# Kernel optimization log

Hardware: AMD Instinct MI355X
Metric: run time of the kernel (lower is better)

The kernel has to match this reference:

```python
import jax, jax.numpy as jnp
import numpy as np

B, S, D, H = 16, 512, 1024, 4096
TOP_K = H // 4  # default: hidden_dim // 4


def setup_inputs() -> dict:
    key = jax.random.key(0)
    ks = jax.random.split(key, 11)
    s = lambda fan_in: 1.0 / np.sqrt(fan_in)
    return {
        "inputs": jax.random.normal(ks[0], (B, S, D), jnp.float32),
        "up_w": jax.random.uniform(ks[1], (H, D), jnp.float32, -s(D), s(D)),
        "up_b": jax.random.uniform(ks[2], (H,), jnp.float32, -s(D), s(D)),
        "gate_w1": jax.random.uniform(ks[3], (H, D), jnp.float32, -s(D), s(D)),
        "gate_b1": jax.random.uniform(ks[4], (H,), jnp.float32, -s(D), s(D)),
        "gate_w2": jax.random.uniform(ks[5], (H, H), jnp.float32, -s(H), s(H)),
        "gate_b2": jax.random.uniform(ks[6], (H,), jnp.float32, -s(H), s(H)),
        "mod_w": jax.random.uniform(ks[7], (H, D), jnp.float32, -s(D), s(D)),
        "mod_b": jax.random.uniform(ks[8], (H,), jnp.float32, -s(D), s(D)),
        "down_w": jax.random.uniform(ks[9], (D, H), jnp.float32, -s(H), s(H)),
        "down_b": jax.random.uniform(ks[10], (D,), jnp.float32, -s(H), s(H)),
    }


def reference(inputs, up_w, up_b, gate_w1, gate_b1, gate_w2, gate_b2,
              mod_w, mod_b, down_w, down_b):
    b, s_len, d = inputs.shape
    h_dim = up_w.shape[0]
    # gate MLP -> scores [B, S, H]
    scores = jax.nn.relu(jnp.einsum('bsd,hd->bsh', inputs, gate_w1) + gate_b1)
    scores = jnp.einsum('bsh,gh->bsg', scores, gate_w2) + gate_b2
    flat = scores.reshape(b, s_len * h_dim)
    k = min(TOP_K * s_len, s_len * h_dim)
    _, flat_idx = jax.lax.top_k(flat, k)                    # [B, k]
    hidden_idx = flat_idx % h_dim                           # [B, k]
    # mask[b, h] = True if row h of up.weight was overwritten by mod.weight
    # (duplicate indices write the same value, so set-semantics are exact)
    mask = jnp.zeros((b, h_dim), bool).at[
        jnp.arange(b)[:, None], hidden_idx].set(True)       # [B, H]
    # Instead of materializing per-batch [B,H,D] weights, compute both shared-
    # weight GEMMs and select per (batch, hidden) row — identical math.
    h_up = jnp.einsum('bsd,hd->bsh', inputs, up_w) + up_b
    h_mod = jnp.einsum('bsd,hd->bsh', inputs, mod_w) + mod_b
    h = jnp.where(mask[:, None, :], h_mod, h_up)            # [B, S, H]
    h = jax.nn.silu(h)
    # dropout is identity in eval/reference mode
    return jnp.einsum('bsh,dh->bsd', h, down_w) + down_b
```

## Files before the change

kernel.cpp:

```cpp
#include <hip/hip_runtime.h>
#include <cstdint>

typedef __attribute__((ext_vector_type(4))) _Float16 f16x4;
typedef __attribute__((ext_vector_type(8))) _Float16 f16x8;
typedef __attribute__((ext_vector_type(4))) float f32x4;

#define D_DIM 1024
#define H_DIM 4096
#define BS_ROWS 8192
#define K_SEL 524288u
#define CAND_CAP 32768u

__device__ __forceinline__ unsigned lkey(float v){
  float u = fmaf(v, 67108864.f, 268435456.f);
  u = fminf(fmaxf(u, 0.f), 536870911.f);
  return (unsigned)u;
}

__device__ __forceinline__ void gload16(const _Float16* g, _Float16* l){
  __builtin_amdgcn_global_load_lds(
      (const __attribute__((address_space(1))) void*)g,
      (__attribute__((address_space(3))) void*)l, 16, 0, 0);
}

template<int N> __device__ __forceinline__ void waitcnt_vm(){
  if      constexpr (N == 0) asm volatile("s_waitcnt vmcnt(0)" ::: "memory");
  else if constexpr (N == 4) asm volatile("s_waitcnt vmcnt(4)" ::: "memory");
  else if constexpr (N == 6) asm volatile("s_waitcnt vmcnt(6)" ::: "memory");
  else                       asm volatile("s_waitcnt vmcnt(8)" ::: "memory");
}

__device__ __forceinline__ size_t img_g32(int row, int k8, int nkt32){
  int p = (row & 127) >> 1;
  int s = (((row & 1) << 2) | (k8 & 3)) ^ (p & 7);
  return ((size_t)((row >> 7) * nkt32 + (k8 >> 2)) << 9) + (p << 3) + s;
}

__global__ __launch_bounds__(256)
void pack_all(const float* __restrict__ X, const float* __restrict__ g1w,
              const float* __restrict__ g2w, const float* __restrict__ upw,
              const float* __restrict__ modw, const float* __restrict__ dww,
              _Float16* __restrict__ Xhi, _Float16* __restrict__ Xlo,
              _Float16* __restrict__ G1hi, _Float16* __restrict__ G1lo,
              _Float16* __restrict__ G2hi, _Float16* __restrict__ G2lo,
              _Float16* __restrict__ UPhi, _Float16* __restrict__ MODhi,
              _Float16* __restrict__ DWhi)
{
  unsigned g = blockIdx.x * 256u + threadIdx.x;
  const float* W; _Float16* hi; _Float16* lo = nullptr;
  int k8s, n32; unsigned base;
  if      (g < 1048576u){ W=X;    hi=Xhi;  lo=Xlo;  k8s=7; n32=32;  base=0u;        }
  else if (g < 1572864u){ W=g1w;  hi=G1hi; lo=G1lo; k8s=7; n32=32;  base=1048576u; }
  else if (g < 3670016u){ W=g2w;  hi=G2hi; lo=G2lo; k8s=9; n32=128; base=1572864u; }
  else if (g < 4194304u){ W=upw;  hi=UPhi;          k8s=7; n32=32;  base=3670016u; }
  else if (g < 4718592u){ W=modw; hi=MODhi;         k8s=7; n32=32;  base=4194304u; }
  else                  { W=dww;  hi=DWhi;          k8s=9; n32=128; base=4718592u; }
  g -= base;
  int row = (int)(g >> k8s), k8 = (int)(g & ((1u << k8s) - 1u));
  const float* src = W + ((size_t)row << (k8s + 3)) + (k8 << 3);
  float4 f0 = *(const float4*)src, f1 = *(const float4*)(src + 4);
  float ff[8] = {f0.x,f0.y,f0.z,f0.w,f1.x,f1.y,f1.z,f1.w};
  f16x8 hv, lv;
  #pragma unroll
  for (int i = 0; i < 8; i++){
    hv[i] = (_Float16)ff[i];
    lv[i] = (_Float16)(ff[i] - (float)hv[i]);
  }
  size_t d = img_g32(row, k8, n32) << 3;
  *(f16x8*)&hi[d] = hv;
  if (lo) *(f16x8*)&lo[d] = lv;
}

enum { MODE_G1 = 0, MODE_G2 = 1, MODE_UPMOD = 2, MODE_DOWN = 3 };

template<int MODE>
__global__ __launch_bounds__(256)
void gemm_t(const _Float16* __restrict__ Ahi, const _Float16* __restrict__ Alo,
            const _Float16* __restrict__ Bhi, const _Float16* __restrict__ Blo,
            const float* __restrict__ bias0, const float* __restrict__ bias1,
            const unsigned* __restrict__ mask,
            _Float16* __restrict__ Chi, _Float16* __restrict__ Clo,
            float* __restrict__ C32,
            int N, int K, int m_img_base, int c_row_base)
{
  constexpr int NSEG = (MODE == MODE_G1) ? 3 : 1;
  constexpr bool BSEL = (MODE == MODE_UPMOD);
  constexpr int NLD = (NSEG == 3) ? 8 : 4;
  constexpr int DEPTH = (NSEG == 3) ? 2 : 3;
  __shared__ __align__(16) _Float16 sA [DEPTH][4096];
  __shared__ __align__(16) _Float16 sB [DEPTH][4096];
  __shared__ __align__(16) _Float16 sAl[NSEG == 3 ? 2 : 1][NSEG == 3 ? 4096 : 8];
  __shared__ __align__(16) _Float16 sBl[NSEG == 3 ? 2 : 1][NSEG == 3 ? 4096 : 8];

  const int nbx = gridDim.x;
  const int h = blockIdx.y * nbx + blockIdx.x;
  const int xcd = h & 7, idx = h >> 3;
  const int cw = nbx >> 2;
  const int ch = gridDim.y >> 1;
  const int bx = (xcd & 3) * cw + idx % cw;
  const int by = (xcd >> 2) * ch + idx / cw;

  const int tid = threadIdx.x;
  const int lane = tid & 63;
  const int w  = tid >> 6;
  const int wr = w >> 1, wc = w & 1;
  const int lr = lane & 15;
  const int q  = lane >> 4;

  const int m0 = m_img_base + by * 128;
  const int n0 = bx * 128;
  const int nkt = K >> 5;
  const size_t arow = (size_t)(m0 >> 7) * nkt;
  const size_t brow = (size_t)(n0 >> 7) * nkt;

  const _Float16* bsrcl[2];
  if (BSEL){
    const int bb = m0 >> 9;
    #pragma unroll
    for (int j = 0; j < 2; j++){
      int gi = (w*2 + j)*64 + lane;
      int p = gi >> 3, x = (gi & 7) ^ (p & 7);
      int row = (p << 1) | (x >> 2);
      bsrcl[j] = (mask[bb * H_DIM + n0 + row] ? Blo : Bhi) + (gi << 3);
    }
    waitcnt_vm<0>();
  }

  f32x4 acc[4][4];
  #pragma unroll
  for (int i = 0; i < 4; i++)
    #pragma unroll
    for (int j = 0; j < 4; j++) acc[i][j] = (f32x4){0.f,0.f,0.f,0.f};

  const int soff = (((((lr & 1) << 2) | q) ^ (lr >> 1)) << 3);

  auto STAGE = [&](int buf, int kt){
    const _Float16* at = Ahi + ((arow + kt) << 12);
    #pragma unroll
    for (int j = 0; j < 2; j++)
      gload16(at + ((w*2 + j) << 9) + (lane << 3), &sA[buf][(w*2 + j) << 9]);
    if (NSEG == 3){
      const _Float16* alt = Alo + ((arow + kt) << 12);
      const _Float16* bht = Bhi + ((brow + kt) << 12);
      const _Float16* blt = Blo + ((brow + kt) << 12);
      #pragma unroll
      for (int j = 0; j < 2; j++){
        gload16(alt + ((w*2 + j) << 9) + (lane << 3), &sAl[buf][(w*2 + j) << 9]);
        gload16(bht + ((w*2 + j) << 9) + (lane << 3), &sB [buf][(w*2 + j) << 9]);
        gload16(blt + ((w*2 + j) << 9) + (lane << 3), &sBl[buf][(w*2 + j) << 9]);
      }
    } else if (BSEL){
      const size_t toff = (brow + kt) << 12;
      #pragma unroll
      for (int j = 0; j < 2; j++)
        gload16(bsrcl[j] + toff, &sB[buf][(w*2 + j) << 9]);
    } else {
      const _Float16* bht = Bhi + ((brow + kt) << 12);
      #pragma unroll
      for (int j = 0; j < 2; j++)
        gload16(bht + ((w*2 + j) << 9) + (lane << 3), &sB[buf][(w*2 + j) << 9]);
    }
  };

  STAGE(0, 0);
  if (DEPTH == 3) STAGE(1, 1);

  for (int kt = 0; kt < nkt; ++kt){
    const int rem = nkt - 1 - kt;
    const int cur = (DEPTH == 2) ? (kt & 1) : (kt % 3);
    if (DEPTH == 2){
      if (rem >= 1){ STAGE((kt + 1) & 1, kt + 1); waitcnt_vm<NLD>(); }
      else         { waitcnt_vm<0>(); }
    } else {
      if (rem >= 2){ STAGE((kt + 2) % 3, kt + 2); waitcnt_vm<8>(); }
      else if (rem == 1){ waitcnt_vm<4>(); }
      else         { waitcnt_vm<0>(); }
    }
    __builtin_amdgcn_s_barrier();
    __builtin_amdgcn_sched_barrier(0);

    f16x8 fah[4], fbh[4], fal[4], fbl[4];
    #pragma unroll
    for (int i = 0; i < 4; i++){
      const int ap = ((wr*32 + i*8 + (lr >> 1)) << 6) + soff;
      const int bp = ((wc*32 + i*8 + (lr >> 1)) << 6) + soff;
      fah[i] = *(const f16x8*)&sA[cur][ap];
      fbh[i] = *(const f16x8*)&sB[cur][bp];
      if (NSEG == 3){
        fal[i] = *(const f16x8*)&sAl[cur][ap];
        fbl[i] = *(const f16x8*)&sBl[cur][bp];
      }
    }
    #pragma unroll
    for (int mi = 0; mi < 4; mi++)
      #pragma unroll
      for (int ni = 0; ni < 4; ni++)
        acc[mi][ni] = __builtin_amdgcn_mfma_f32_16x16x32_f16(fah[mi], fbh[ni], acc[mi][ni], 0,0,0);
    if (NSEG == 3){
      #pragma unroll
      for (int mi = 0; mi < 4; mi++)
        #pragma unroll
        for (int ni = 0; ni < 4; ni++)
          acc[mi][ni] = __builtin_amdgcn_mfma_f32_16x16x32_f16(fal[mi], fbh[ni], acc[mi][ni], 0,0,0);
      #pragma unroll
      for (int mi = 0; mi < 4; mi++)
        #pragma unroll
        for (int ni = 0; ni < 4; ni++)
          acc[mi][ni] = __builtin_amdgcn_mfma_f32_16x16x32_f16(fah[mi], fbl[ni], acc[mi][ni], 0,0,0);
    }
    __builtin_amdgcn_s_barrier();
  }

  #pragma unroll
  for (int ni = 0; ni < 4; ni++){
    const int gc = n0 + wc*64 + ni*16 + lr;
    float bias;
    if (MODE == MODE_UPMOD) bias = mask[(m0 >> 9) * H_DIM + gc] ? bias1[gc] : bias0[gc];
    else                    bias = bias0[gc];
    #pragma unroll
    for (int mi = 0; mi < 4; mi++){
      #pragma unroll
      for (int r = 0; r < 4; r++){
        const int gr = m0 + wr*64 + mi*16 + q*4 + r;
        const int cr = gr - c_row_base;
        float v = acc[mi][ni][r] + bias;
        if (MODE == MODE_G1){
          v = fmaxf(v, 0.f);
          size_t d = (img_g32(cr, gc >> 3, N >> 5) << 3) + (gc & 7);
          Chi[d] = (_Float16)v;
        }
        if (MODE == MODE_UPMOD){
          v = v / (1.f + __expf(-v));
          size_t d = (img_g32(cr, gc >> 3, N >> 5) << 3) + (gc & 7);
          Chi[d] = (_Float16)v;
        }
        if (MODE == MODE_DOWN) C32[(size_t)cr * N + gc] = v;
      }
    }
  }
}

__global__ __launch_bounds__(512, 1)
void gemm_g1(const _Float16* __restrict__ Ahi, const _Float16* __restrict__ Alo,
             const _Float16* __restrict__ Bhi, const _Float16* __restrict__ Blo,
             const float* __restrict__ bias0, _Float16* __restrict__ Chi,
             int N, int K, int m_img_base, int c_row_base)
{
  __shared__ __align__(16) _Float16 sAh[3][8192];
  __shared__ __align__(16) _Float16 sAl[3][8192];
  __shared__ __align__(16) _Float16 sBh[3][4096];
  __shared__ __align__(16) _Float16 sBl[3][4096];

  const int nbx = gridDim.x;
  const int h = blockIdx.y * nbx + blockIdx.x;
  const int xcd = h & 7, idx = h >> 3;
  const int cw = nbx >> 2, ch = gridDim.y >> 1;
  const int bx = (xcd & 3) * cw + idx % cw;
  const int by = (xcd >> 2) * ch + idx / cw;

  const int tid = threadIdx.x;
  const int lane = tid & 63;
  const int w = tid >> 6;
  const int wrow = w >> 1, wcol = w & 1;
  const int lr = lane & 15;
  const int q = lane >> 4;

  const int m0 = m_img_base + by * 256;
  const int n0 = bx * 128;
  const int nkt = K >> 5;
  const int at0 = (m0 >> 7) * nkt;
  const int bt0 = (n0 >> 7) * nkt;

  f32x4 acc[4][4];
  #pragma unroll
  for (int i = 0; i < 4; i++)
    #pragma unroll
    for (int j = 0; j < 4; j++) acc[i][j] = (f32x4){0.f,0.f,0.f,0.f};

  const int soff = (((((lr & 1) << 2) | q) ^ (lr >> 1)) << 3);
  int offA[4], offB[4];
  #pragma unroll
  for (int mi = 0; mi < 4; mi++)
    offA[mi] = (wrow >> 1)*4096 + ((((wrow & 1)*32) + mi*8 + (lr >> 1)) << 6) + soff;
  #pragma unroll
  for (int ni = 0; ni < 4; ni++)
    offB[ni] = ((wcol*32 + ni*8 + (lr >> 1)) << 6) + soff;

  auto STA = [&](int buf, int rb, int kt, bool lo){
    const _Float16* img = lo ? Alo : Ahi;
    _Float16* dst = (lo ? &sAl[buf][0] : &sAh[buf][0]) + rb*4096 + (tid << 3);
    gload16(img + ((((size_t)(at0 + rb*nkt + kt)) << 9) + tid) * 8, dst);
  };
  auto STB = [&](int buf, int kt, bool lo){
    const _Float16* img = lo ? Blo : Bhi;
    _Float16* dst = (lo ? &sBl[buf][0] : &sBh[buf][0]) + (tid << 3);
    gload16(img + ((((size_t)(bt0 + kt)) << 9) + tid) * 8, dst);
  };

#define G1PHASE(P, STG)                                                        \
  {                                                                            \
    f16x8 ah = *(const f16x8*)&sAh[cur][offA[P]];                              \
    f16x8 al = *(const f16x8*)&sAl[cur][offA[P]];                              \
    STG;                                                                       \
    if ((P) == 3){ if (pf) waitcnt_vm<6>(); else waitcnt_vm<0>(); }            \
    __builtin_amdgcn_s_barrier();                                              \
    asm volatile("s_waitcnt lgkmcnt(0)" ::: "memory");                         \
    __builtin_amdgcn_sched_barrier(0);                                         \
    __builtin_amdgcn_s_setprio(1);                                             \
    _Pragma("unroll")                                                          \
    for (int ni = 0; ni < 4; ni++)                                             \
      acc[P][ni] = __builtin_amdgcn_mfma_f32_16x16x32_f16(ah, fbh[ni], acc[P][ni], 0,0,0); \
    _Pragma("unroll")                                                          \
    for (int ni = 0; ni < 4; ni++)                                             \
      acc[P][ni] = __builtin_amdgcn_mfma_f32_16x16x32_f16(al, fbh[ni], acc[P][ni], 0,0,0); \
    _Pragma("unroll")                                                          \
    for (int ni = 0; ni < 4; ni++)                                             \
      acc[P][ni] = __builtin_amdgcn_mfma_f32_16x16x32_f16(ah, fbl[ni], acc[P][ni], 0,0,0); \
    __builtin_amdgcn_s_setprio(0);                                             \
    __builtin_amdgcn_s_barrier();                                              \
  }

  STA(0,0,0,false); STA(0,1,0,false); STA(0,0,0,true); STA(0,1,0,true);
  STB(0,0,false);   STB(0,0,true);
  STA(1,0,1,false); STA(1,1,1,false); STA(1,0,1,true); STA(1,1,1,true);
  STB(1,1,false);   STB(1,1,true);
  waitcnt_vm<6>();
  __builtin_amdgcn_s_barrier();

  for (int kt = 0; kt < nkt; ++kt){
    const int cur = kt % 3, nb = (kt + 2) % 3;
    const bool pf = (kt + 2 < nkt);
    f16x8 fbh[4], fbl[4];
    #pragma unroll
    for (int ni = 0; ni < 4; ni++){
      fbh[ni] = *(const f16x8*)&sBh[cur][offB[ni]];
      fbl[ni] = *(const f16x8*)&sBl[cur][offB[ni]];
    }
    G1PHASE(0, if (pf){ STA(nb,0,kt+2,false); STA(nb,1,kt+2,false); })
    G1PHASE(1, if (pf){ STA(nb,0,kt+2,true);  STA(nb,1,kt+2,true);  })
    G1PHASE(2, if (pf){ STB(nb,kt+2,false);   STB(nb,kt+2,true);    })
    G1PHASE(3, )
  }
#undef G1PHASE

  #pragma unroll
  for (int ni = 0; ni < 4; ni++){
    const int gc = n0 + wcol*64 + ni*16 + lr;
    const float bias = bias0[gc];
    #pragma unroll
    for (int mi = 0; mi < 4; mi++){
      #pragma unroll
      for (int r = 0; r < 4; r++){
        const int gr = m0 + wrow*64 + mi*16 + q*4 + r;
        const int cr = gr - c_row_base;
        float v = fmaxf(acc[mi][ni][r] + bias, 0.f);
        size_t d = (img_g32(cr, gc >> 3, N >> 5) << 3) + (gc & 7);
        Chi[d] = (_Float16)v;
      }
    }
  }
}

__global__ __launch_bounds__(512, 2)
void gemm_g2(const _Float16* __restrict__ A, const _Float16* __restrict__ B,
             const float* __restrict__ bias0,
             unsigned* __restrict__ keys, unsigned* __restrict__ Mkey,
             unsigned* __restrict__ hist, int N, int K, int batch_base)
{
  __shared__ __align__(16) _Float16 sAb[3][8192];
  __shared__ __align__(16) _Float16 sBb[3][8192];

  const int nbx = gridDim.x;
  const int h = blockIdx.y * nbx + blockIdx.x;
  const int xcd = h & 7, idx = h >> 3;
  const int cw = nbx >> 2, ch = gridDim.y >> 1;
  const int bx = (xcd & 3) * cw + idx % cw;
  const int by = (xcd >> 2) * ch + idx / cw;

  const int tid = threadIdx.x;
  const int lane = tid & 63;
  const int w = tid >> 6;
  const int wrow = w >> 2, wcol = w & 3;
  const int lr = lane & 15;
  const int q = lane >> 4;

  const int m0 = by * 256;
  const int n0 = bx * 256;
  const int nkt = K >> 5;
  const int ar0 = (m0 >> 7) * nkt;
  const int br0 = (n0 >> 7) * nkt;

  f32x4 acc[8][4];
  #pragma unroll
  for (int i = 0; i < 8; i++)
    #pragma unroll
    for (int j = 0; j < 4; j++) acc[i][j] = (f32x4){0.f,0.f,0.f,0.f};

  const int soff = (((((lr & 1) << 2) | q) ^ (lr >> 1)) << 3);
  int offA[8], offB[4];
  #pragma unroll
  for (int mi = 0; mi < 8; mi++) offA[mi] = ((mi*8 + (lr >> 1)) << 6) + soff;
  #pragma unroll
  for (int ni = 0; ni < 4; ni++)
    offB[ni] = (((wcol & 1)*32 + ni*8 + (lr >> 1)) << 6) + soff;
  const int arb = wrow * 4096;
  const int bcb = (wcol >> 1) * 4096;

  auto STA = [&](int buf, int rb, int kt){
    gload16(A + ((((size_t)(ar0 + rb*nkt + kt) << 9) + tid) << 3),
            &sAb[buf][rb*4096 + (tid << 3)]);
  };
  auto STB = [&](int buf, int cb, int kt){
    gload16(B + ((((size_t)(br0 + cb*nkt + kt) << 9) + tid) << 3),
            &sBb[buf][cb*4096 + (tid << 3)]);
  };

#define G2PHASE(P, STG)                                                        \
  {                                                                            \
    f16x8 a0 = *(const f16x8*)&sAb[cur][arb + offA[2*(P)]];                    \
    f16x8 a1 = *(const f16x8*)&sAb[cur][arb + offA[2*(P)+1]];                  \
    STG;                                                                       \
    if ((P) == 3){ if (pf) waitcnt_vm<4>(); else waitcnt_vm<0>(); }            \
    __builtin_amdgcn_s_barrier();                                              \
    asm volatile("s_waitcnt lgkmcnt(0)" ::: "memory");                         \
    __builtin_amdgcn_sched_barrier(0);                                         \
    __builtin_amdgcn_s_setprio(1);                                             \
    _Pragma("unroll")                                                          \
    for (int ni = 0; ni < 4; ni++)                                             \
      acc[2*(P)][ni]   = __builtin_amdgcn_mfma_f32_16x16x32_f16(a0, fb[ni], acc[2*(P)][ni], 0,0,0);   \
    _Pragma("unroll")                                                          \
    for (int ni = 0; ni < 4; ni++)                                             \
      acc[2*(P)+1][ni] = __builtin_amdgcn_mfma_f32_16x16x32_f16(a1, fb[ni], acc[2*(P)+1][ni], 0,0,0); \
    __builtin_amdgcn_s_setprio(0);                                             \
    __builtin_amdgcn_s_barrier();                                              \
  }

  STA(0,0,0); STB(0,0,0); STB(0,1,0); STA(0,1,0);
  STA(1,0,1); STB(1,0,1); STB(1,1,1); STA(1,1,1);
  waitcnt_vm<4>();
  __builtin_amdgcn_s_barrier();

  for (int kt = 0; kt < nkt; ++kt){
    const int cur = kt % 3, nb = (kt + 2) % 3;
    const bool pf = (kt + 2 < nkt);
    f16x8 fb[4];
    #pragma unroll
    for (int ni = 0; ni < 4; ni++)
      fb[ni] = *(const f16x8*)&sBb[cur][bcb + offB[ni]];
    G2PHASE(0, if (pf) STA(nb, 0, kt+2))
    G2PHASE(1, if (pf) STB(nb, 0, kt+2))
    G2PHASE(2, if (pf) STB(nb, 1, kt+2))
    G2PHASE(3, if (pf) STA(nb, 1, kt+2))
  }
#undef G2PHASE

  unsigned* lh = (unsigned*)&sAb[0][0];
  __syncthreads();
  for (int i = tid; i < 4096; i += 512) lh[i] = 0;
  __syncthreads();

  const int gb = batch_base + (m0 >> 9);
  #pragma unroll
  for (int ni = 0; ni < 4; ni++){
    const int gc = n0 + wcol*64 + ni*16 + lr;
    const float bias = bias0[gc];
    unsigned colmax = 0u;
    #pragma unroll
    for (int mi = 0; mi < 8; mi++){
      #pragma unroll
      for (int r = 0; r < 4; r++){
        const int gr = m0 + wrow*128 + mi*16 + q*4 + r;
        float v = acc[mi][ni][r] + bias;
        unsigned key = lkey(v);
        keys[(size_t)gr * N + gc] = key;
        colmax = max(colmax, key);
        atomicAdd(&lh[key >> 17], 1u);
      }
    }
    atomicMax(&Mkey[gb * H_DIM + gc], colmax);
  }
  __syncthreads();
  for (int i = tid; i < 4096; i += 512)
    if (lh[i]) atomicAdd(&hist[(gb << 12) + i], lh[i]);
}


__global__ __launch_bounds__(256)
void select12(const unsigned* __restrict__ hist, unsigned* __restrict__ b12,
              unsigned* __restrict__ krem, unsigned* __restrict__ ccount, int b0)
{
  const int b = b0 + (int)blockIdx.x;
  __shared__ unsigned part[256];
  const unsigned base = (unsigned)b << 12;
  unsigned s = 0;
  #pragma unroll
  for (int i = 0; i < 16; i++) s += hist[base + threadIdx.x*16 + i];
  part[threadIdx.x] = s;
  __syncthreads();
  if (threadIdx.x == 0){
    unsigned cum = 0; int t = 255;
    for (; t > 0; --t){
      if (cum + part[t] >= K_SEL) break;
      cum += part[t];
    }
    int bin = 15; unsigned kr = K_SEL;
    for (; bin > 0; --bin){
      unsigned c = hist[base + t*16 + bin];
      if (cum + c >= K_SEL) break;
      cum += c;
    }
    kr = K_SEL - cum;
    b12[b] = (unsigned)(t*16 + bin);
    krem[b] = kr;
    ccount[b] = 0;
  }
}

__global__ __launch_bounds__(256)
void collect(const unsigned* __restrict__ keys, const unsigned* __restrict__ b12,
             unsigned* __restrict__ cand, unsigned* __restrict__ ccount, int b0)
{
  __shared__ unsigned cbuf[1024];
  __shared__ unsigned lcnt, gbase;
  const int bl = blockIdx.y;
  const int b  = b0 + bl;
  const unsigned bin = b12[b];
  if (threadIdx.x == 0) lcnt = 0;
  __syncthreads();
  const uint4* p = (const uint4*)(keys + (size_t)bl*2097152u + (size_t)blockIdx.x*8192u);
  uint4 kv[8];
  #pragma unroll
  for (int j = 0; j < 8; j++) kv[j] = p[threadIdx.x + j*256];
  #pragma unroll
  for (int j = 0; j < 8; j++){
    #pragma unroll
    for (int e = 0; e < 4; e++){
      unsigned k = (e==0)?kv[j].x:(e==1)?kv[j].y:(e==2)?kv[j].z:kv[j].w;
      if ((k >> 17) == bin){
        unsigned idx = atomicAdd(&lcnt, 1u);
        if (idx < 1024u) cbuf[idx] = k;
      }
    }
  }
  __syncthreads();
  const unsigned n = lcnt < 1024u ? lcnt : 1024u;
  if (threadIdx.x == 0) gbase = atomicAdd(&ccount[b], n);
  __syncthreads();
  const unsigned gb = gbase;
  for (unsigned i = threadIdx.x; i < n; i += 256){
    unsigned dst = gb + i;
    if (dst < CAND_CAP) cand[((size_t)b << 15) + dst] = cbuf[i];
  }
}

__global__ __launch_bounds__(256)
void select_exact(const unsigned* __restrict__ cand, const unsigned* __restrict__ ccount,
                  const unsigned* __restrict__ b12, const unsigned* __restrict__ kremA,
                  unsigned* __restrict__ tkey, int b0)
{
  const int b = b0 + (int)blockIdx.x;
  unsigned cc = ccount[b];
  const unsigned n = cc < CAND_CAP ? cc : CAND_CAP;
  __shared__ unsigned h[256];
  __shared__ unsigned sh2[2];
  unsigned prefix = b12[b] << 17;
  unsigned krem = kremA[b];
  const unsigned pm[3]  = {0xFFFE0000u, 0xFFFFFE00u, 0xFFFFFFFEu};
  const int      shs[3] = {9, 1, 0};
  const int      wid[3] = {256, 256, 2};
  for (int pass = 0; pass < 3; ++pass){
    if (threadIdx.x < (unsigned)wid[pass]) h[threadIdx.x] = 0;
    __syncthreads();
    for (unsigned i = threadIdx.x; i < n; i += 256){
      unsigned k = cand[((size_t)b << 15) + i];
      if ((k & pm[pass]) == prefix)
        atomicAdd(&h[(k >> shs[pass]) & (unsigned)(wid[pass]-1)], 1u);
    }
    __syncthreads();
    if (threadIdx.x == 0){
      unsigned cum = 0; int bin = wid[pass]-1;
      for (; bin > 0; --bin){
        unsigned c = h[bin];
        if (cum + c >= krem) break;
        cum += c;
      }
      krem -= cum;
      prefix |= ((unsigned)bin) << shs[pass];
      sh2[0] = prefix; sh2[1] = krem;
    }
    __syncthreads();
    prefix = sh2[0]; krem = sh2[1];
    __syncthreads();
  }
  if (threadIdx.x == 0) tkey[b] = prefix;
}

__global__ __launch_bounds__(256)
void make_mask(const unsigned* __restrict__ Mkey, const unsigned* __restrict__ tkey,
               unsigned* __restrict__ mask){
  const int i = blockIdx.x * 256 + threadIdx.x;
  const int b = i >> 12;
  mask[i] = (Mkey[i] >= tkey[b]) ? 1u : 0u;
}

extern "C" void kernel_launch(void* const* d_in, const int* in_sizes, int n_in,
                              void* d_out, int out_size, void* d_ws, size_t ws_size,
                              hipStream_t stream)
{
  (void)in_sizes; (void)n_in; (void)out_size; (void)ws_size;
  const float* X      = (const float*)d_in[0];
  const float* up_w   = (const float*)d_in[1];
  const float* up_b   = (const float*)d_in[2];
  const float* g1w    = (const float*)d_in[3];
  const float* g1b    = (const float*)d_in[4];
  const float* g2w    = (const float*)d_in[5];
  const float* g2b    = (const float*)d_in[6];
  const float* mod_w  = (const float*)d_in[7];
  const float* mod_b  = (const float*)d_in[8];
  const float* down_w = (const float*)d_in[9];
  const float* down_b = (const float*)d_in[10];
  float* out = (float*)d_out;

  char* ws = (char*)d_ws;
  _Float16* Xhi  = (_Float16*)(ws);
  _Float16* Xlo  = (_Float16*)(ws + (16ull<<20));
  _Float16* G1hi = (_Float16*)(ws + (32ull<<20));
  _Float16* G1lo = (_Float16*)(ws + (40ull<<20));
  _Float16* G2hi = (_Float16*)(ws + (48ull<<20));
  _Float16* UPhi = (_Float16*)(ws + (112ull<<20));
  _Float16* MODhi= (_Float16*)(ws + (120ull<<20));
  _Float16* DWhi = (_Float16*)(ws + (128ull<<20));
  _Float16* Fhi  = (_Float16*)(ws + (136ull<<20));
  unsigned* keys = (unsigned*)(ws + (168ull<<20));
  _Float16* Hbuf = (_Float16*)(ws + (136ull<<20));
  char* aux = ws + (232ull<<20);
  unsigned* Mkey  = (unsigned*)(aux);
  unsigned* maskb = (unsigned*)(aux + 262144);
  unsigned* hist  = (unsigned*)(aux + 524288);
  unsigned* cand  = (unsigned*)(aux + 786432);
  unsigned* b12   = (unsigned*)(aux + 786432 + 2097152);
  unsigned* krem  = (unsigned*)(aux + 786432 + 2097152 + 64);
  unsigned* ccnt  = (unsigned*)(aux + 786432 + 2097152 + 128);
  unsigned* tkey  = (unsigned*)(aux + 786432 + 2097152 + 192);

  pack_all<<<20480, 256, 0, stream>>>(X, g1w, g2w, up_w, mod_w, down_w,
                                      Xhi, Xlo, G1hi, G1lo, G2hi, nullptr,
                                      UPhi, MODhi, DWhi);

  hipMemsetAsync(Mkey, 0, 262144, stream);
  hipMemsetAsync(hist, 0, 262144, stream);

  for (int half = 0; half < 2; ++half){
    const int b0 = half * 8;
    gemm_g1<<<dim3(32, 16), 512, 0, stream>>>(
        Xhi, Xlo, G1hi, G1lo, g1b, Fhi, H_DIM, D_DIM, half*4096, half*4096);
    gemm_g2<<<dim3(16, 16), 512, 0, stream>>>(
        Fhi, G2hi, g2b, keys, Mkey, hist, H_DIM, H_DIM, b0);
    select12<<<8, 256, 0, stream>>>(hist, b12, krem, ccnt, b0);
    collect<<<dim3(256, 8), 256, 0, stream>>>(keys, b12, cand, ccnt, b0);
    select_exact<<<8, 256, 0, stream>>>(cand, ccnt, b12, krem, tkey, b0);
  }
  make_mask<<<256, 256, 0, stream>>>(Mkey, tkey, maskb);

  gemm_t<MODE_UPMOD><<<dim3(32, 64), 256, 0, stream>>>(
      Xhi, nullptr, UPhi, MODhi, up_b, mod_b, maskb,
      Hbuf, nullptr, nullptr, H_DIM, D_DIM, 0, 0);
  gemm_t<MODE_DOWN><<<dim3(8, 64), 256, 0, stream>>>(
      Hbuf, nullptr, DWhi, nullptr, down_b, nullptr, nullptr,
      nullptr, nullptr, out, D_DIM, H_DIM, 0, 0);
}
```

Measured before the change: 934.2 us.

## Restructure gate-1 split-fp16 GEMM as virtual 3x-K loop with 256x256 tiles

```diff
diff --git a/kernel.cpp b/kernel.cpp
--- a/kernel.cpp
+++ b/kernel.cpp
@@ -241,15 +241,13 @@
 }
 
 __global__ __launch_bounds__(512, 1)
-void gemm_g1(const _Float16* __restrict__ Ahi, const _Float16* __restrict__ Alo,
-             const _Float16* __restrict__ Bhi, const _Float16* __restrict__ Blo,
-             const float* __restrict__ bias0, _Float16* __restrict__ Chi,
-             int N, int K, int m_img_base, int c_row_base)
-{
-  __shared__ __align__(16) _Float16 sAh[3][8192];
-  __shared__ __align__(16) _Float16 sAl[3][8192];
-  __shared__ __align__(16) _Float16 sBh[3][4096];
-  __shared__ __align__(16) _Float16 sBl[3][4096];
+void gemm_g1v(const _Float16* __restrict__ Ahi, const _Float16* __restrict__ Alo,
+              const _Float16* __restrict__ Bhi, const _Float16* __restrict__ Blo,
+              const float* __restrict__ bias0, _Float16* __restrict__ Chi,
+              int N, int K, int m_img_base, int c_row_base)
+{
+  __shared__ __align__(16) _Float16 sAb[3][8192];
+  __shared__ __align__(16) _Float16 sBb[3][8192];
 
   const int nbx = gridDim.x;
   const int h = blockIdx.y * nbx + blockIdx.x;
@@ -261,97 +259,94 @@
   const int tid = threadIdx.x;
   const int lane = tid & 63;
   const int w = tid >> 6;
-  const int wrow = w >> 1, wcol = w & 1;
+  const int wrow = w >> 2, wcol = w & 3;
   const int lr = lane & 15;
   const int q = lane >> 4;
 
   const int m0 = m_img_base + by * 256;
-  const int n0 = bx * 128;
-  const int nkt = K >> 5;
-  const int at0 = (m0 >> 7) * nkt;
-  const int bt0 = (n0 >> 7) * nkt;
-
-  f32x4 acc[4][4];
-  #pragma unroll
-  for (int i = 0; i < 4; i++)
+  const int n0 = bx * 256;
+  const int nks = K >> 5;
+  const int nkt = 3 * nks;
+  const int ar0 = (m0 >> 7) * nks;
+  const int br0 = (n0 >> 7) * nks;
+
+  f32x4 acc[8][4];
+  #pragma unroll
+  for (int i = 0; i < 8; i++)
     #pragma unroll
     for (int j = 0; j < 4; j++) acc[i][j] = (f32x4){0.f,0.f,0.f,0.f};
 
   const int soff = (((((lr & 1) << 2) | q) ^ (lr >> 1)) << 3);
-  int offA[4], offB[4];
-  #pragma unroll
-  for (int mi = 0; mi < 4; mi++)
-    offA[mi] = (wrow >> 1)*4096 + ((((wrow & 1)*32) + mi*8 + (lr >> 1)) << 6) + soff;
+  int offA[8], offB[4];
+  #pragma unroll
+  for (int mi = 0; mi < 8; mi++) offA[mi] = ((mi*8 + (lr >> 1)) << 6) + soff;
   #pragma unroll
   for (int ni = 0; ni < 4; ni++)
-    offB[ni] = ((wcol*32 + ni*8 + (lr >> 1)) << 6) + soff;
-
-  auto STA = [&](int buf, int rb, int kt, bool lo){
-    const _Float16* img = lo ? Alo : Ahi;
-    _Float16* dst = (lo ? &sAl[buf][0] : &sAh[buf][0]) + rb*4096 + (tid << 3);
-    gload16(img + ((((size_t)(at0 + rb*nkt + kt)) << 9) + tid) * 8, dst);
+    offB[ni] = (((wcol & 1)*32 + ni*8 + (lr >> 1)) << 6) + soff;
+  const int arb = wrow * 4096;
+  const int bcb = (wcol >> 1) * 4096;
+
+  auto STA = [&](int buf, int rb, int kt){
+    const int seg = kt >> 5, lk = kt & 31;
+    const _Float16* img = (seg == 1) ? Alo : Ahi;
+    gload16(img + ((((size_t)(ar0 + rb*nks + lk) << 9) + tid) << 3),
+            &sAb[buf][rb*4096 + (tid << 3)]);
   };
-  auto STB = [&](int buf, int kt, bool lo){
-    const _Float16* img = lo ? Blo : Bhi;
-    _Float16* dst = (lo ? &sBl[buf][0] : &sBh[buf][0]) + (tid << 3);
-    gload16(img + ((((size_t)(bt0 + kt)) << 9) + tid) * 8, dst);
+  auto STB = [&](int buf, int cb, int kt){
+    const int seg = kt >> 5, lk = kt & 31;
+    const _Float16* img = (seg == 2) ? Blo : Bhi;
+    gload16(img + ((((size_t)(br0 + cb*nks + lk) << 9) + tid) << 3),
+            &sBb[buf][cb*4096 + (tid << 3)]);
   };
 
-#define G1PHASE(P, STG)                                                        \
+#define G1VPHASE(P, STG)                                                       \
   {                                                                            \
-    f16x8 ah = *(const f16x8*)&sAh[cur][offA[P]];                              \
-    f16x8 al = *(const f16x8*)&sAl[cur][offA[P]];                              \
+    f16x8 a0 = *(const f16x8*)&sAb[cur][arb + offA[2*(P)]];                    \
+    f16x8 a1 = *(const f16x8*)&sAb[cur][arb + offA[2*(P)+1]];                  \
     STG;                                                                       \
-    if ((P) == 3){ if (pf) waitcnt_vm<6>(); else waitcnt_vm<0>(); }            \
+    if ((P) == 3){ if (pf) waitcnt_vm<4>(); else waitcnt_vm<0>(); }            \
     __builtin_amdgcn_s_barrier();                                              \
     asm volatile("s_waitcnt lgkmcnt(0)" ::: "memory");                         \
     __builtin_amdgcn_sched_barrier(0);                                         \
     __builtin_amdgcn_s_setprio(1);                                             \
     _Pragma("unroll")                                                          \
     for (int ni = 0; ni < 4; ni++)                                             \
-      acc[P][ni] = __builtin_amdgcn_mfma_f32_16x16x32_f16(ah, fbh[ni], acc[P][ni], 0,0,0); \
+      acc[2*(P)][ni]   = __builtin_amdgcn_mfma_f32_16x16x32_f16(a0, fb[ni], acc[2*(P)][ni], 0,0,0);   \
     _Pragma("unroll")                                                          \
     for (int ni = 0; ni < 4; ni++)                                             \
-      acc[P][ni] = __builtin_amdgcn_mfma_f32_16x16x32_f16(al, fbh[ni], acc[P][ni], 0,0,0); \
-    _Pragma("unroll")                                                          \
-    for (int ni = 0; ni < 4; ni++)                                             \
-      acc[P][ni] = __builtin_amdgcn_mfma_f32_16x16x32_f16(ah, fbl[ni], acc[P][ni], 0,0,0); \
+      acc[2*(P)+1][ni] = __builtin_amdgcn_mfma_f32_16x16x32_f16(a1, fb[ni], acc[2*(P)+1][ni], 0,0,0); \
     __builtin_amdgcn_s_setprio(0);                                             \
     __builtin_amdgcn_s_barrier();                                              \
   }
 
-  STA(0,0,0,false); STA(0,1,0,false); STA(0,0,0,true); STA(0,1,0,true);
-  STB(0,0,false);   STB(0,0,true);
-  STA(1,0,1,false); STA(1,1,1,false); STA(1,0,1,true); STA(1,1,1,true);
-  STB(1,1,false);   STB(1,1,true);
-  waitcnt_vm<6>();
+  STA(0,0,0); STB(0,0,0); STB(0,1,0); STA(0,1,0);
+  STA(1,0,1); STB(1,0,1); STB(1,1,1); STA(1,1,1);
+  waitcnt_vm<4>();
   __builtin_amdgcn_s_barrier();
 
   for (int kt = 0; kt < nkt; ++kt){
     const int cur = kt % 3, nb = (kt + 2) % 3;
     const bool pf = (kt + 2 < nkt);
-    f16x8 fbh[4], fbl[4];
-    #pragma unroll
-    for (int ni = 0; ni < 4; ni++){
-      fbh[ni] = *(const f16x8*)&sBh[cur][offB[ni]];
-      fbl[ni] = *(const f16x8*)&sBl[cur][offB[ni]];
-    }
-    G1PHASE(0, if (pf){ STA(nb,0,kt+2,false); STA(nb,1,kt+2,false); })
-    G1PHASE(1, if (pf){ STA(nb,0,kt+2,true);  STA(nb,1,kt+2,true);  })
-    G1PHASE(2, if (pf){ STB(nb,kt+2,false);   STB(nb,kt+2,true);    })
-    G1PHASE(3, )
-  }
-#undef G1PHASE
+    f16x8 fb[4];
+    #pragma unroll
+    for (int ni = 0; ni < 4; ni++)
+      fb[ni] = *(const f16x8*)&sBb[cur][bcb + offB[ni]];
+    G1VPHASE(0, if (pf) STA(nb, 0, kt+2))
+    G1VPHASE(1, if (pf) STB(nb, 0, kt+2))
+    G1VPHASE(2, if (pf) STB(nb, 1, kt+2))
+    G1VPHASE(3, if (pf) STA(nb, 1, kt+2))
+  }
+#undef G1VPHASE
 
   #pragma unroll
   for (int ni = 0; ni < 4; ni++){
     const int gc = n0 + wcol*64 + ni*16 + lr;
     const float bias = bias0[gc];
     #pragma unroll
-    for (int mi = 0; mi < 4; mi++){
+    for (int mi = 0; mi < 8; mi++){
       #pragma unroll
       for (int r = 0; r < 4; r++){
-        const int gr = m0 + wrow*64 + mi*16 + q*4 + r;
+        const int gr = m0 + wrow*128 + mi*16 + q*4 + r;
         const int cr = gr - c_row_base;
         float v = fmaxf(acc[mi][ni][r] + bias, 0.f);
         size_t d = (img_g32(cr, gc >> 3, N >> 5) << 3) + (gc & 7);
@@ -652,7 +647,7 @@
 
   for (int half = 0; half < 2; ++half){
     const int b0 = half * 8;
-    gemm_g1<<<dim3(32, 16), 512, 0, stream>>>(
+    gemm_g1v<<<dim3(16, 16), 512, 0, stream>>>(
         Xhi, Xlo, G1hi, G1lo, g1b, Fhi, H_DIM, D_DIM, half*4096, half*4096);
     gemm_g2<<<dim3(16, 16), 512, 0, stream>>>(
         Fhi, G2hi, g2b, keys, Mkey, hist, H_DIM, H_DIM, b0);
```

After: 977.7 us. 4.7% more time.
